# Optimization experiments

Hardware: AMD Instinct MI355X
Metric: run time of the kernel (lower is better)

Reference implementation:

```python
import jax, jax.numpy as jnp
import numpy as np

D_IN = 128
D_K = 100
SCALE = float(np.sqrt(100.0))


def setup_inputs() -> dict:
    key = jax.random.key(0)
    ks = jax.random.split(key, 8)
    S = 8192
    x1 = jax.random.uniform(ks[0], (S, D_IN), dtype=jnp.float32)
    x2 = jax.random.uniform(ks[1], (S, D_IN), dtype=jnp.float32)
    # Linear params (PyTorch Linear: y = x @ W.T + b); stored here pre-transposed as [in, out]
    lim = 1.0 / np.sqrt(D_IN)
    Wq = jax.random.uniform(ks[2], (D_IN, D_K), jnp.float32, -lim, lim)
    bq = jax.random.uniform(ks[3], (D_K,), jnp.float32, -lim, lim)
    Wk = jax.random.uniform(ks[4], (D_IN, D_K), jnp.float32, -lim, lim)
    bk = jax.random.uniform(ks[5], (D_K,), jnp.float32, -lim, lim)
    Wv = jax.random.uniform(ks[6], (D_IN, D_K), jnp.float32, -lim, lim)
    bv = jax.random.uniform(ks[7], (D_K,), jnp.float32, -lim, lim)
    return {"x1": x1, "x2": x2, "Wq": Wq, "bq": bq, "Wk": Wk, "bk": bk, "Wv": Wv, "bv": bv}


def reference(x1, x2, Wq, bq, Wk, bk, Wv, bv):
    # Q/K/V projections
    q = x1 @ Wq + bq          # [S, D_K]
    k = x2 @ Wk + bk          # [S, D_K]
    v = x2 @ Wv + bv          # [S, D_K]
    # scaled dot-product attention (single head); dropout is identity (eval mode)
    scores = jnp.einsum('qd,kd->qk', q, k) / SCALE   # [S, S]
    attn = jax.nn.softmax(scores, axis=-1)
    return attn @ v            # [S, D_K]
```

## Files before the change

kernel.cpp:

```cpp
#include <hip/hip_runtime.h>
#include <hip/hip_bf16.h>


typedef __bf16 bf16x8 __attribute__((ext_vector_type(8)));
typedef float  f32x4  __attribute__((ext_vector_type(4)));
typedef short  short8_t __attribute__((ext_vector_type(8)));

#define SM_C 0.14426950408889634f

#if __has_builtin(__builtin_amdgcn_global_load_lds)
#define HAVE_GLL 1
#endif

__device__ __forceinline__ void gload16(const short* g, short* l){
#ifdef HAVE_GLL
  __builtin_amdgcn_global_load_lds(
      (__attribute__((address_space(1))) void*)g,
      (__attribute__((address_space(3))) void*)l,
      16, 0, 0);
#else
  *(short8_t*)(l + (threadIdx.x & 63)*8) = *(const short8_t*)(g);
#endif
}

__device__ __forceinline__ short bf(float f){ return __builtin_bit_cast(short, (__bf16)f); }

__global__ __launch_bounds__(256) void proj_qkv(
    const float* __restrict__ x1, const float* __restrict__ x2,
    const float* __restrict__ Wq, const float* __restrict__ bq,
    const float* __restrict__ Wk, const float* __restrict__ bk,
    const float* __restrict__ Wv, const float* __restrict__ bv,
    short* __restrict__ qg, short* __restrict__ kg, short* __restrict__ vT2)
{
  __shared__ float xs[16][128];
  __shared__ float vs[16][104];
  const int z = blockIdx.y;
  const float* x = (z == 0) ? x1 : x2;
  const float* W = (z == 0) ? Wq : (z == 1) ? Wk : Wv;
  const float* b = (z == 0) ? bq : (z == 1) ? bk : bv;
  const int rb = blockIdx.x << 4;
  const int t  = threadIdx.x;
  for (int i = t; i < 2048; i += 256) xs[i >> 7][i & 127] = x[(rb << 7) + i];
  __syncthreads();
  const int rw = t >> 5, cs = t & 31;
  float4 a0 = make_float4(0.f,0.f,0.f,0.f), a1 = a0;
  if (cs < 25){
    a0 = *(const float4*)(b + (cs << 2)); a1 = a0;
#pragma unroll 8
    for (int i = 0; i < 128; ++i){
      const float4 wv = *(const float4*)(W + i*100 + (cs << 2));
      const float xv0 = xs[rw][i], xv1 = xs[rw+8][i];
      a0.x = fmaf(xv0, wv.x, a0.x); a0.y = fmaf(xv0, wv.y, a0.y);
      a0.z = fmaf(xv0, wv.z, a0.z); a0.w = fmaf(xv0, wv.w, a0.w);
      a1.x = fmaf(xv1, wv.x, a1.x); a1.y = fmaf(xv1, wv.y, a1.y);
      a1.z = fmaf(xv1, wv.z, a1.z); a1.w = fmaf(xv1, wv.w, a1.w);
    }
  }
  if (z < 2){
    short* o = (z == 0) ? qg : kg;
    if (cs < 25){
      short4 h0, h1;
      h0.x=bf(a0.x); h0.y=bf(a0.y); h0.z=bf(a0.z); h0.w=bf(a0.w);
      h1.x=bf(a1.x); h1.y=bf(a1.y); h1.z=bf(a1.z); h1.w=bf(a1.w);
      *(short4*)(o + ((rb + rw)     << 7) + (cs << 2)) = h0;
      *(short4*)(o + ((rb + rw + 8) << 7) + (cs << 2)) = h1;
    } else {
      short4 hz; hz.x=0; hz.y=0; hz.z=0; hz.w=0;
      *(short4*)(o + ((rb + rw)     << 7) + 100 + ((cs - 25) << 2)) = hz;
      *(short4*)(o + ((rb + rw + 8) << 7) + 100 + ((cs - 25) << 2)) = hz;
    }
  } else {
    if (cs < 25){
      vs[rw  ][(cs<<2)+0]=a0.x; vs[rw  ][(cs<<2)+1]=a0.y; vs[rw  ][(cs<<2)+2]=a0.z; vs[rw  ][(cs<<2)+3]=a0.w;
      vs[rw+8][(cs<<2)+0]=a1.x; vs[rw+8][(cs<<2)+1]=a1.y; vs[rw+8][(cs<<2)+2]=a1.z; vs[rw+8][(cs<<2)+3]=a1.w;
    }
    __syncthreads();
    if (t < 128){
      const int d = t;
#pragma unroll
      for (int h = 0; h < 4; ++h){
        const int kv0 = rb + h*4;
        const int o32 = kv0 & 31;
        const int idx = (o32 < 16) ? ((o32 >> 2) << 3) : ((((o32 - 16) >> 2) << 3) + 4);
        short4 hv;
        float f0 = (d<100)? vs[(kv0  )-rb+0>0? (kv0-rb):(kv0-rb)][d] : 0.f; (void)f0;
        const int r0 = kv0 - rb;
        hv.x = (d<100)? bf(vs[r0+0][d]) : (short)0;
        hv.y = (d<100)? bf(vs[r0+1][d]) : (short)0;
        hv.z = (d<100)? bf(vs[r0+2][d]) : (short)0;
        hv.w = (d<100)? bf(vs[r0+3][d]) : (short)0;
        *(short4*)(vT2 + (d << 13) + (kv0 & ~63) + ((kv0 >> 5) & 1)*32 + idx) = hv;
      }
    }
  }
}

__global__ __launch_bounds__(256, 2) void attn_fwd(
    const short* __restrict__ qg, const short* __restrict__ kg,
    const short* __restrict__ vT2, float* __restrict__ pacc,
    float2* __restrict__ pml)
{
  __shared__ alignas(16) short sK[2][64*128];
  __shared__ alignas(16) short sVT[2][112*64];
  const int tid  = threadIdx.x;
  const int w    = tid >> 6;
  const int lane = tid & 63;
  const int g    = lane >> 4;
  const int ln   = lane & 15;
  const int qt   = blockIdx.x & 63;
  const int part = blockIdx.x >> 6;
  const int qb   = qt*128 + w*32;

  bf16x8 qf[2][4];
#pragma unroll
  for (int sub = 0; sub < 2; ++sub)
#pragma unroll
    for (int ks = 0; ks < 4; ++ks)
      qf[sub][ks] = *(const bf16x8*)(qg + (qb + sub*16 + ln)*128 + ks*32 + g*8);

  f32x4 acc[2][7];
#pragma unroll
  for (int sub = 0; sub < 2; ++sub)
#pragma unroll
    for (int db = 0; db < 7; ++db) acc[sub][db] = f32x4{0.f,0.f,0.f,0.f};
  float mrun[2] = {-3.0e38f, -3.0e38f};
  float lsum[2] = {0.f, 0.f};

  auto stage = [&](int kv0, int buf){
#pragma unroll
    for (int i = 0; i < 4; ++i){
      const int id = w + (i << 2);
      const int r  = (id << 2) + (lane >> 4);
      const int bx = (lane & 15) ^ (r & 15);
      gload16(kg + (kv0 + r)*128 + bx*8, &sK[buf][id << 9]);
    }
#pragma unroll
    for (int i = 0; i < 3; ++i){
      const int id = w + (i << 2);
      const int r  = (id << 3) + (lane >> 3);
      const int bx = (lane & 7) ^ (r & 7);
      gload16(vT2 + r*8192 + kv0 + bx*8, &sVT[buf][id << 9]);
    }
    if (w < 2){
      const int id = 12 + w;
      const int r  = (id << 3) + (lane >> 3);
      const int bx = (lane & 7) ^ (r & 7);
      gload16(vT2 + r*8192 + kv0 + bx*8, &sVT[buf][id << 9]);
    }
  };

  const int kvbase = part << 10;
  stage(kvbase, 0);
  int cur = 0;
  for (int t = 0; t < 16; ++t){
    __syncthreads();
    if (t < 15) stage(kvbase + ((t+1) << 6), cur ^ 1);
    const short* sKc = sK[cur];
    const short* sVc = sVT[cur];

    f32x4 st[2][4];
#pragma unroll
    for (int s = 0; s < 4; ++s){ st[0][s] = f32x4{0.f,0.f,0.f,0.f}; st[1][s] = f32x4{0.f,0.f,0.f,0.f}; }
#pragma unroll
    for (int s = 0; s < 4; ++s){
      const int rbase = (s*16 + ln) << 7;
#pragma unroll
      for (int ks = 0; ks < 4; ++ks){
        bf16x8 kf = *(const bf16x8*)(sKc + rbase + ((((ks<<2) + g) ^ ln) << 3));
        st[0][s] = __builtin_amdgcn_mfma_f32_16x16x32_bf16(kf, qf[0][ks], st[0][s], 0, 0, 0);
        st[1][s] = __builtin_amdgcn_mfma_f32_16x16x32_bf16(kf, qf[1][ks], st[1][s], 0, 0, 0);
      }
    }

    bf16x8 pb[2][2];
#pragma unroll
    for (int sub = 0; sub < 2; ++sub){
      float mx = st[sub][0][0];
#pragma unroll
      for (int s = 0; s < 4; ++s)
#pragma unroll
        for (int r = 0; r < 4; ++r) mx = fmaxf(mx, st[sub][s][r]);
      mx = fmaxf(mx, __shfl_xor(mx, 16));
      mx = fmaxf(mx, __shfl_xor(mx, 32));
      if (!__all(mx - mrun[sub] <= 8.0f)){
        const float mnew = fmaxf(mrun[sub], mx);
        const float f = exp2f((mrun[sub] - mnew) * SM_C);
        lsum[sub] *= f;
#pragma unroll
        for (int db = 0; db < 7; ++db) acc[sub][db] *= f;
        mrun[sub] = mnew;
      }
      const float mc = mrun[sub] * SM_C;
      float p[4][4]; float ps = 0.f;
#pragma unroll
      for (int s = 0; s < 4; ++s)
#pragma unroll
        for (int r = 0; r < 4; ++r){
          p[s][r] = exp2f(fmaf(st[sub][s][r], SM_C, -mc));
          ps += p[s][r];
        }
      lsum[sub] += ps;
#pragma unroll
      for (int c = 0; c < 2; ++c){
        bf16x8 pv;
#pragma unroll
        for (int r = 0; r < 4; ++r){
          pv[r]   = (__bf16)p[2*c][r];
          pv[4+r] = (__bf16)p[2*c+1][r];
        }
        pb[sub][c] = pv;
      }
    }

#pragma unroll
    for (int c = 0; c < 2; ++c)
#pragma unroll
      for (int db = 0; db < 7; ++db){
        const int row = db*16 + ln;
        bf16x8 vf = *(const bf16x8*)(sVc + (row << 6) + (((((c<<2) + g)) ^ (ln & 7)) << 3));
        acc[0][db] = __builtin_amdgcn_mfma_f32_16x16x32_bf16(vf, pb[0][c], acc[0][db], 0, 0, 0);
        acc[1][db] = __builtin_amdgcn_mfma_f32_16x16x32_bf16(vf, pb[1][c], acc[1][db], 0, 0, 0);
      }
    cur ^= 1;
  }

#pragma unroll
  for (int sub = 0; sub < 2; ++sub){
    float ls = lsum[sub];
    ls += __shfl_xor(ls, 16);
    ls += __shfl_xor(ls, 32);
    lsum[sub] = ls;
  }
#pragma unroll
  for (int sub = 0; sub < 2; ++sub)
#pragma unroll
    for (int db = 0; db < 7; ++db)
#pragma unroll
      for (int r = 0; r < 4; ++r){
        const int d = db*16 + g*4 + r;
        if (d < 100)
          pacc[((part*100 + d) << 13) + qb + sub*16 + ln] = acc[sub][db][r];
      }
  if (g == 0) pml[(part << 13) + qb + ln]      = make_float2(mrun[0], lsum[0]);
  if (g == 1) pml[(part << 13) + qb + 16 + ln] = make_float2(mrun[1], lsum[1]);
}

__global__ __launch_bounds__(256) void merge_parts(
    const float* __restrict__ pacc, const float2* __restrict__ pml,
    float* __restrict__ out)
{
  __shared__ float ol[64][21];
  const int t  = threadIdx.x;
  const int tq = t & 63;
  const int td = t >> 6;
  const int qb = blockIdx.x << 6;
  const int db = blockIdx.y * 20;
  const int q  = qb + tq;
  float m8[8], l8[8];
  float mstar = -3.0e38f;
#pragma unroll
  for (int p = 0; p < 8; ++p){
    float2 ml = pml[(p << 13) + q];
    m8[p] = ml.x; l8[p] = ml.y;
    mstar = fmaxf(mstar, ml.x);
  }
  float L = 0.f; float w8[8];
#pragma unroll
  for (int p = 0; p < 8; ++p){ w8[p] = exp2f((m8[p] - mstar) * SM_C); L += l8[p]*w8[p]; }
  const float inv = 1.0f / L;
#pragma unroll
  for (int i = 0; i < 5; ++i){
    const int d = db + td*5 + i;
    float s = 0.f;
#pragma unroll
    for (int p = 0; p < 8; ++p) s += pacc[((p*100 + d) << 13) + q] * w8[p];
    ol[tq][td*5 + i] = s * inv;
  }
  __syncthreads();
  for (int idx = t; idx < 1280; idx += 256){
    const int q2 = idx / 20, d2 = idx - q2*20;
    out[(qb + q2)*100 + db + d2] = ol[q2][d2];
  }
}

extern "C" void kernel_launch(void* const* d_in, const int* in_sizes, int n_in,
                              void* d_out, int out_size, void* d_ws, size_t ws_size,
                              hipStream_t stream)
{
  const float* x1 = (const float*)d_in[0];
  const float* x2 = (const float*)d_in[1];
  const float* Wq = (const float*)d_in[2];
  const float* bq = (const float*)d_in[3];
  const float* Wk = (const float*)d_in[4];
  const float* bk = (const float*)d_in[5];
  const float* Wv = (const float*)d_in[6];
  const float* bv = (const float*)d_in[7];
  char* ws = (char*)d_ws;
  short*  qg   = (short*)ws;
  short*  kg   = (short*)(ws + (1u << 21));
  short*  vT2  = (short*)(ws + (2u << 21));
  float*  pacc = (float*)(ws + (3u << 21));
  float2* pml  = (float2*)(ws + (3u << 21) + 8u*100u*8192u*4u);
  float*  out  = (float*)d_out;

  proj_qkv<<<dim3(512, 3), 256, 0, stream>>>(x1, x2, Wq, bq, Wk, bk, Wv, bv, qg, kg, vT2);
  attn_fwd<<<512, 256, 0, stream>>>(qg, kg, vT2, pacc, pml);
  merge_parts<<<dim3(128, 5), 256, 0, stream>>>(pacc, pml, out);
}
```

Baseline: 84.57 us.

## Split KV into 16 parts with 32-key tiles, bf16 partials, higher occupancy

Doubles the KV split from 8 to 16 parts (1024 blocks) and halves the KV tile to 32 keys. This shrinks LDS and register use so the kernel can declare 4 blocks per CU, and it relayouts the transposed V to a padded 40-element row stride. Partial accumulators are stored as bf16 to cut workspace traffic, and setprio is wrapped around the MFMA sections. The cost is twice as many softmax-rescale passes per key, a larger merge over 16 partials, and precision loss from bf16 partial sums.

```diff
diff --git a/kernel.cpp b/kernel.cpp
--- a/kernel.cpp
+++ b/kernel.cpp
@@ -24,6 +24,10 @@
 }
 
 __device__ __forceinline__ short bf(float f){ return __builtin_bit_cast(short, (__bf16)f); }
+__device__ __forceinline__ float bf2f(unsigned short v){
+  unsigned u = ((unsigned)v) << 16;
+  return __builtin_bit_cast(float, u);
+}
 
 __global__ __launch_bounds__(256) void proj_qkv(
     const float* __restrict__ x1, const float* __restrict__ x2,
@@ -82,26 +86,25 @@
         const int kv0 = rb + h*4;
         const int o32 = kv0 & 31;
         const int idx = (o32 < 16) ? ((o32 >> 2) << 3) : ((((o32 - 16) >> 2) << 3) + 4);
+        const int r0 = kv0 - rb;
         short4 hv;
-        float f0 = (d<100)? vs[(kv0  )-rb+0>0? (kv0-rb):(kv0-rb)][d] : 0.f; (void)f0;
-        const int r0 = kv0 - rb;
         hv.x = (d<100)? bf(vs[r0+0][d]) : (short)0;
         hv.y = (d<100)? bf(vs[r0+1][d]) : (short)0;
         hv.z = (d<100)? bf(vs[r0+2][d]) : (short)0;
         hv.w = (d<100)? bf(vs[r0+3][d]) : (short)0;
-        *(short4*)(vT2 + (d << 13) + (kv0 & ~63) + ((kv0 >> 5) & 1)*32 + idx) = hv;
-      }
-    }
-  }
-}
-
-__global__ __launch_bounds__(256, 2) void attn_fwd(
+        *(short4*)(vT2 + (d << 13) + (kv0 & ~31) + idx) = hv;
+      }
+    }
+  }
+}
+
+__global__ __launch_bounds__(256, 4) void attn_fwd(
     const short* __restrict__ qg, const short* __restrict__ kg,
-    const short* __restrict__ vT2, float* __restrict__ pacc,
+    const short* __restrict__ vT2, short* __restrict__ pacc,
     float2* __restrict__ pml)
 {
-  __shared__ alignas(16) short sK[2][64*128];
-  __shared__ alignas(16) short sVT[2][112*64];
+  __shared__ alignas(1024) short sK[2][32*128];
+  __shared__ alignas(1024) short sVT[2][4608];
   const int tid  = threadIdx.x;
   const int w    = tid >> 6;
   const int lane = tid & 63;
@@ -128,41 +131,40 @@
 
   auto stage = [&](int kv0, int buf){
 #pragma unroll
-    for (int i = 0; i < 4; ++i){
-      const int id = w + (i << 2);
-      const int r  = (id << 2) + (lane >> 4);
-      const int bx = (lane & 15) ^ (r & 15);
-      gload16(kg + (kv0 + r)*128 + bx*8, &sK[buf][id << 9]);
+    for (int i = 0; i < 2; ++i){
+      const int cid = w + (i << 2);
+      const int r   = (cid << 2) + (lane >> 4);
+      const int bx  = (lane & 15) ^ (r & 15);
+      gload16(kg + (kv0 + r)*128 + bx*8, &sK[buf][cid << 9]);
     }
 #pragma unroll
     for (int i = 0; i < 3; ++i){
-      const int id = w + (i << 2);
-      const int r  = (id << 3) + (lane >> 3);
-      const int bx = (lane & 7) ^ (r & 7);
-      gload16(vT2 + r*8192 + kv0 + bx*8, &sVT[buf][id << 9]);
-    }
-    if (w < 2){
-      const int id = 12 + w;
-      const int r  = (id << 3) + (lane >> 3);
-      const int bx = (lane & 7) ^ (r & 7);
-      gload16(vT2 + r*8192 + kv0 + bx*8, &sVT[buf][id << 9]);
+      const int cid = w + (i << 2);
+      if (cid < 9){
+        const int a = (cid << 10) + (lane << 4);
+        const int r = a / 80;
+        const int m = (a - r*80) >> 4;
+        const int srcm = (m == 4) ? 0 : m;
+        gload16(vT2 + r*8192 + kv0 + srcm*8, &sVT[buf][cid << 9]);
+      }
     }
   };
 
-  const int kvbase = part << 10;
+  const int kvbase = part << 9;
   stage(kvbase, 0);
   int cur = 0;
   for (int t = 0; t < 16; ++t){
     __syncthreads();
-    if (t < 15) stage(kvbase + ((t+1) << 6), cur ^ 1);
+    if (t < 15) stage(kvbase + ((t+1) << 5), cur ^ 1);
     const short* sKc = sK[cur];
     const short* sVc = sVT[cur];
 
-    f32x4 st[2][4];
-#pragma unroll
-    for (int s = 0; s < 4; ++s){ st[0][s] = f32x4{0.f,0.f,0.f,0.f}; st[1][s] = f32x4{0.f,0.f,0.f,0.f}; }
-#pragma unroll
-    for (int s = 0; s < 4; ++s){
+    f32x4 st[2][2];
+#pragma unroll
+    for (int s = 0; s < 2; ++s){ st[0][s] = f32x4{0.f,0.f,0.f,0.f}; st[1][s] = f32x4{0.f,0.f,0.f,0.f}; }
+    __builtin_amdgcn_s_setprio(1);
+#pragma unroll
+    for (int s = 0; s < 2; ++s){
       const int rbase = (s*16 + ln) << 7;
 #pragma unroll
       for (int ks = 0; ks < 4; ++ks){
@@ -171,13 +173,14 @@
         st[1][s] = __builtin_amdgcn_mfma_f32_16x16x32_bf16(kf, qf[1][ks], st[1][s], 0, 0, 0);
       }
     }
-
-    bf16x8 pb[2][2];
+    __builtin_amdgcn_s_setprio(0);
+
+    bf16x8 pb[2];
 #pragma unroll
     for (int sub = 0; sub < 2; ++sub){
       float mx = st[sub][0][0];
 #pragma unroll
-      for (int s = 0; s < 4; ++s)
+      for (int s = 0; s < 2; ++s)
 #pragma unroll
         for (int r = 0; r < 4; ++r) mx = fmaxf(mx, st[sub][s][r]);
       mx = fmaxf(mx, __shfl_xor(mx, 16));
@@ -191,36 +194,33 @@
         mrun[sub] = mnew;
       }
       const float mc = mrun[sub] * SM_C;
-      float p[4][4]; float ps = 0.f;
-#pragma unroll
-      for (int s = 0; s < 4; ++s)
+      float p[2][4]; float ps = 0.f;
+#pragma unroll
+      for (int s = 0; s < 2; ++s)
 #pragma unroll
         for (int r = 0; r < 4; ++r){
           p[s][r] = exp2f(fmaf(st[sub][s][r], SM_C, -mc));
           ps += p[s][r];
         }
       lsum[sub] += ps;
-#pragma unroll
-      for (int c = 0; c < 2; ++c){
-        bf16x8 pv;
-#pragma unroll
-        for (int r = 0; r < 4; ++r){
-          pv[r]   = (__bf16)p[2*c][r];
-          pv[4+r] = (__bf16)p[2*c+1][r];
-        }
-        pb[sub][c] = pv;
-      }
-    }
-
-#pragma unroll
-    for (int c = 0; c < 2; ++c)
-#pragma unroll
-      for (int db = 0; db < 7; ++db){
-        const int row = db*16 + ln;
-        bf16x8 vf = *(const bf16x8*)(sVc + (row << 6) + (((((c<<2) + g)) ^ (ln & 7)) << 3));
-        acc[0][db] = __builtin_amdgcn_mfma_f32_16x16x32_bf16(vf, pb[0][c], acc[0][db], 0, 0, 0);
-        acc[1][db] = __builtin_amdgcn_mfma_f32_16x16x32_bf16(vf, pb[1][c], acc[1][db], 0, 0, 0);
-      }
+      bf16x8 pv;
+#pragma unroll
+      for (int r = 0; r < 4; ++r){
+        pv[r]   = (__bf16)p[0][r];
+        pv[4+r] = (__bf16)p[1][r];
+      }
+      pb[sub] = pv;
+    }
+
+    __builtin_amdgcn_s_setprio(1);
+#pragma unroll
+    for (int db = 0; db < 7; ++db){
+      const int row = db*16 + ln;
+      bf16x8 vf = *(const bf16x8*)(sVc + row*40 + (g << 3));
+      acc[0][db] = __builtin_amdgcn_mfma_f32_16x16x32_bf16(vf, pb[0], acc[0][db], 0, 0, 0);
+      acc[1][db] = __builtin_amdgcn_mfma_f32_16x16x32_bf16(vf, pb[1], acc[1][db], 0, 0, 0);
+    }
+    __builtin_amdgcn_s_setprio(0);
     cur ^= 1;
   }
 
@@ -239,14 +239,14 @@
       for (int r = 0; r < 4; ++r){
         const int d = db*16 + g*4 + r;
         if (d < 100)
-          pacc[((part*100 + d) << 13) + qb + sub*16 + ln] = acc[sub][db][r];
+          pacc[((part*100 + d) << 13) + qb + sub*16 + ln] = bf(acc[sub][db][r]);
       }
   if (g == 0) pml[(part << 13) + qb + ln]      = make_float2(mrun[0], lsum[0]);
   if (g == 1) pml[(part << 13) + qb + 16 + ln] = make_float2(mrun[1], lsum[1]);
 }
 
 __global__ __launch_bounds__(256) void merge_parts(
-    const float* __restrict__ pacc, const float2* __restrict__ pml,
+    const short* __restrict__ pacc, const float2* __restrict__ pml,
     float* __restrict__ out)
 {
   __shared__ float ol[64][21];
@@ -256,24 +256,25 @@
   const int qb = blockIdx.x << 6;
   const int db = blockIdx.y * 20;
   const int q  = qb + tq;
-  float m8[8], l8[8];
+  float m16[16], l16[16];
   float mstar = -3.0e38f;
 #pragma unroll
-  for (int p = 0; p < 8; ++p){
+  for (int p = 0; p < 16; ++p){
     float2 ml = pml[(p << 13) + q];
-    m8[p] = ml.x; l8[p] = ml.y;
+    m16[p] = ml.x; l16[p] = ml.y;
     mstar = fmaxf(mstar, ml.x);
   }
-  float L = 0.f; float w8[8];
-#pragma unroll
-  for (int p = 0; p < 8; ++p){ w8[p] = exp2f((m8[p] - mstar) * SM_C); L += l8[p]*w8[p]; }
+  float L = 0.f; float w16[16];
+#pragma unroll
+  for (int p = 0; p < 16; ++p){ w16[p] = exp2f((m16[p] - mstar) * SM_C); L += l16[p]*w16[p]; }
   const float inv = 1.0f / L;
 #pragma unroll
   for (int i = 0; i < 5; ++i){
     const int d = db + td*5 + i;
     float s = 0.f;
 #pragma unroll
-    for (int p = 0; p < 8; ++p) s += pacc[((p*100 + d) << 13) + q] * w8[p];
+    for (int p = 0; p < 16; ++p)
+      s += bf2f((unsigned short)pacc[((p*100 + d) << 13) + q]) * w16[p];
     ol[tq][td*5 + i] = s * inv;
   }
   __syncthreads();
@@ -299,11 +300,11 @@
   short*  qg   = (short*)ws;
   short*  kg   = (short*)(ws + (1u << 21));
   short*  vT2  = (short*)(ws + (2u << 21));
-  float*  pacc = (float*)(ws + (3u << 21));
-  float2* pml  = (float2*)(ws + (3u << 21) + 8u*100u*8192u*4u);
+  short*  pacc = (short*)(ws + (3u << 21));
+  float2* pml  = (float2*)(ws + (3u << 21) + 16u*100u*8192u*2u);
   float*  out  = (float*)d_out;
 
   proj_qkv<<<dim3(512, 3), 256, 0, stream>>>(x1, x2, Wq, bq, Wk, bk, Wv, bv, qg, kg, vT2);
-  attn_fwd<<<512, 256, 0, stream>>>(qg, kg, vT2, pacc, pml);
+  attn_fwd<<<1024, 256, 0, stream>>>(qg, kg, vT2, pacc, pml);
   merge_parts<<<dim3(128, 5), 256, 0, stream>>>(pacc, pml, out);
 }
```

New measurement: 97.40 us. 15.2% more time.
